# Kernel tuning notes

Measured on AMD Instinct MI355X. Metric: run time of the kernel, lower is better.

The kernel has to match this reference:

```python
import jax, jax.numpy as jnp
import numpy as np

HIDDEN = 4096
N_HEADS = 32
N_KV_HEADS = 8
HEAD_DIM = HIDDEN // N_HEADS  # 128
ROPE_THETA = 500000.0
B, S = 1, 2048


def setup_inputs() -> dict:
    key = jax.random.key(0)
    k1, k2, k3, k4, k5 = jax.random.split(key, 5)
    scale = 0.02
    return {
        "hidden_states": jax.random.normal(k1, (B, S, HIDDEN), dtype=jnp.float32),
        "Wq": jax.random.normal(k2, (N_HEADS * HEAD_DIM, HIDDEN), dtype=jnp.float32) * scale,
        "Wk": jax.random.normal(k3, (N_KV_HEADS * HEAD_DIM, HIDDEN), dtype=jnp.float32) * scale,
        "Wv": jax.random.normal(k4, (N_KV_HEADS * HEAD_DIM, HIDDEN), dtype=jnp.float32) * scale,
        "Wo": jax.random.normal(k5, (HIDDEN, N_HEADS * HEAD_DIM), dtype=jnp.float32) * scale,
    }


def _rope_cos_sin(seq_len, head_dim, theta, dtype):
    inv_freq = 1.0 / (theta ** (jnp.arange(0, head_dim, 2, dtype=jnp.float32) / head_dim))  # [hd/2]
    pos = jnp.arange(seq_len, dtype=jnp.float32)
    freqs = jnp.outer(pos, inv_freq)                      # [S, hd/2]
    emb = jnp.concatenate([freqs, freqs], axis=-1)        # [S, hd]
    return jnp.cos(emb).astype(dtype), jnp.sin(emb).astype(dtype)


def _rotate_half(x):
    x1, x2 = jnp.split(x, 2, axis=-1)
    return jnp.concatenate([-x2, x1], axis=-1)


def _apply_rope(x, cos, sin):
    # x: [B, H, S, hd]; cos/sin: [S, hd]
    return x * cos[None, None] + _rotate_half(x) * sin[None, None]


def reference(hidden_states, Wq, Wk, Wv, Wo):
    b, s, _ = hidden_states.shape
    groups = N_HEADS // N_KV_HEADS

    # fused QKV projections (Linear with weight [out, in])
    q = jnp.einsum("bsd,ed->bse", hidden_states, Wq).reshape(b, s, N_HEADS, HEAD_DIM).transpose(0, 2, 1, 3)
    k = jnp.einsum("bsd,ed->bse", hidden_states, Wk).reshape(b, s, N_KV_HEADS, HEAD_DIM).transpose(0, 2, 1, 3)
    v = jnp.einsum("bsd,ed->bse", hidden_states, Wv).reshape(b, s, N_KV_HEADS, HEAD_DIM).transpose(0, 2, 1, 3)

    cos, sin = _rope_cos_sin(s, HEAD_DIM, ROPE_THETA, hidden_states.dtype)
    q = _apply_rope(q, cos, sin)
    k = _apply_rope(k, cos, sin)

    # GQA: repeat kv heads across groups
    k = jnp.repeat(k, groups, axis=1)  # [B, N_HEADS, S, hd]
    v = jnp.repeat(v, groups, axis=1)

    scale = 1.0 / jnp.sqrt(jnp.asarray(HEAD_DIM, dtype=hidden_states.dtype))
    scores = jnp.einsum("bhqd,bhkd->bhqk", q, k) * scale  # [B, H, S, S]
    causal = jnp.tril(jnp.ones((s, s), dtype=bool))
    scores = jnp.where(causal[None, None], scores, jnp.asarray(-1e30, dtype=scores.dtype))
    attn = jax.nn.softmax(scores, axis=-1)

    out = jnp.einsum("bhqk,bhkd->bhqd", attn, v)          # [B, H, S, hd]
    out = out.transpose(0, 2, 1, 3).reshape(b, s, N_HEADS * HEAD_DIM)
    return jnp.einsum("bse,de->bsd", out, Wo)             # [B, S, HIDDEN]
```

## Files before the change

### kernel.cpp

```cpp
#include <hip/hip_runtime.h>

typedef __attribute__((ext_vector_type(8))) short bf16x8;
typedef __attribute__((ext_vector_type(4))) short bf16x4;
typedef __attribute__((ext_vector_type(4))) float f32x4;
typedef __attribute__((ext_vector_type(16))) float f32x16;

#define S_LEN  2048
#define HID    4096
#define NHEADS 32
#define NKVH   8
#define HDIM   128
#define QKVN   (HID + 2*NKVH*HDIM)
#define KOFS   HID
#define VOFS   (HID + NKVH*HDIM)

#define AS1 __attribute__((address_space(1)))
#define AS3 __attribute__((address_space(3)))

__device__ __forceinline__ unsigned short f2bf(float f){
  unsigned int x = __float_as_uint(f);
  x += 0x7fffu + ((x >> 16) & 1u);
  return (unsigned short)(x >> 16);
}
__device__ __forceinline__ float bf2f(unsigned short h){
  return __uint_as_float(((unsigned int)h) << 16);
}

__global__ void cvt_all(const float* __restrict__ hs, const float* __restrict__ wq,
                        const float* __restrict__ wk, const float* __restrict__ wv,
                        const float* __restrict__ wo,
                        unsigned short* __restrict__ Hb,
                        unsigned short* __restrict__ Wqkvb,
                        unsigned short* __restrict__ Wob){
  const int total = 12582912;
  for (int i = blockIdx.x * blockDim.x + threadIdx.x; i < total; i += gridDim.x * blockDim.x){
    const float* src; unsigned short* dst;
    if (i < 2097152)      { src = hs + (size_t)i*4;             dst = Hb    + (size_t)i*4; }
    else if (i < 6291456) { size_t l = i - 2097152;  src = wq + l*4; dst = Wqkvb + l*4; }
    else if (i < 7340032) { size_t l = i - 6291456;  src = wk + l*4; dst = Wqkvb + 16777216 + l*4; }
    else if (i < 8388608) { size_t l = i - 7340032;  src = wv + l*4; dst = Wqkvb + 20971520 + l*4; }
    else                  { size_t l = i - 8388608;  src = wo + l*4; dst = Wob   + l*4; }
    float4 v = *(const float4*)src;
    ushort4 o;
    o.x = f2bf(v.x); o.y = f2bf(v.y); o.z = f2bf(v.z); o.w = f2bf(v.w);
    *(ushort4*)dst = o;
  }
}

__global__ void rope_table(float* __restrict__ cosT, float* __restrict__ sinT){
  int idx = blockIdx.x * blockDim.x + threadIdx.x;
  int s = idx >> 6, i = idx & 63;
  float inv = expf(-(float)i * (13.122363377404329f / 64.0f));
  float a = (float)s * inv;
  cosT[idx] = cosf(a);
  sinT[idx] = sinf(a);
}

__global__ void rope_apply2(unsigned short* __restrict__ X, const float* __restrict__ cosT,
                            const float* __restrict__ sinT){
  const int totQ = S_LEN*NHEADS*64;
  const int total = totQ + S_LEN*NKVH*64;
  int idx = blockIdx.x * blockDim.x + threadIdx.x;
  if (idx >= total) return;
  int nh, colofs, local;
  if (idx < totQ){ nh = NHEADS; colofs = 0;    local = idx; }
  else           { nh = NKVH;   colofs = KOFS; local = idx - totQ; }
  int i = local & 63;
  int h = (local >> 6) % nh;
  int s = local / (64*nh);
  size_t base = (size_t)s*QKVN + colofs + h*HDIM + i;
  float x0 = bf2f(X[base]), x1 = bf2f(X[base+64]);
  float c = cosT[(s<<6)|i], sn = sinT[(s<<6)|i];
  X[base]    = f2bf(x0*c - x1*sn);
  X[base+64] = f2bf(x1*c + x0*sn);
}

__global__ __launch_bounds__(256) void transpose_v(const unsigned short* __restrict__ QKV,
                                                   unsigned short* __restrict__ Vt){
  __shared__ unsigned short T[64][130];
  const int qt = blockIdx.x, kvh = blockIdx.y;
  const int tid = threadIdx.x;
  #pragma unroll
  for (int i=0;i<4;i++){
    int c = tid + i*256;
    int sl = c >> 4;
    int d0 = (c & 15) * 8;
    bf16x8 v = *(const bf16x8*)&QKV[(size_t)(qt*64+sl)*QKVN + VOFS + kvh*HDIM + d0];
    #pragma unroll
    for (int j=0;j<8;j++) T[sl][d0+j] = (unsigned short)v[j];
  }
  __syncthreads();
  #pragma unroll
  for (int i=0;i<4;i++){
    int c = tid + i*256;
    int d = c >> 3;
    int p0 = (c & 7) * 8;
    bf16x8 o;
    #pragma unroll
    for (int j=0;j<8;j++) o[j] = (short)T[p0+j][d];
    *(bf16x8*)&Vt[((size_t)kvh*HDIM + d)*S_LEN + qt*64 + p0] = o;
  }
}

template<int BM, int BN, int WM, int WN, int OUTF32>
__global__ __launch_bounds__(256, 2) void gemm_fr(const unsigned short* __restrict__ A,
                                                  const unsigned short* __restrict__ W,
                                                  void* __restrict__ C, int M, int N, int K){
  constexpr int MF = (BM/WM)/16;
  constexpr int NF = (BN/WN)/16;
  constexpr int LA = BM/32;
  constexpr int LB = BN/32;
  constexpr int ABYTES = BM*128;
  constexpr int BBYTES = BN*128;
  __shared__ char lds_raw[2*ABYTES + 2*BBYTES];

  const int tid = threadIdx.x;
  const int lane = tid & 63, wv = tid >> 6;
  const int wm = wv / WN, wn = wv % WN;
  const int r = lane & 15, kq = lane >> 4;
  const int tn = blockIdx.x, tm = blockIdx.y;
  const unsigned short* Ab = A + (size_t)tm*BM*K;
  const unsigned short* Wb = W + (size_t)tn*BN*K;

  f32x4 acc[MF][NF];
  #pragma unroll
  for (int m=0;m<MF;m++)
    #pragma unroll
    for (int n=0;n<NF;n++) acc[m][n] = {0.f,0.f,0.f,0.f};

  auto swz = [](int row)->int { return ((row>>1)&3)<<1; };

  auto stage = [&](int buf, int kt){
    #pragma unroll
    for (int l=0;l<LA;l++){
      int c = l*256 + tid;
      int row = c >> 3, ch = c & 7;
      __builtin_amdgcn_global_load_lds(
        (const AS1 void*)(Ab + (size_t)row*K + kt + ((ch ^ swz(row))*8)),
        (AS3 void*)(lds_raw + buf*ABYTES + (l*256 + wv*64)*16), 16, 0, 0);
    }
    #pragma unroll
    for (int l=0;l<LB;l++){
      int c = l*256 + tid;
      int row = c >> 3, ch = c & 7;
      __builtin_amdgcn_global_load_lds(
        (const AS1 void*)(Wb + (size_t)row*K + kt + ((ch ^ swz(row))*8)),
        (AS3 void*)(lds_raw + 2*ABYTES + buf*BBYTES + (l*256 + wv*64)*16), 16, 0, 0);
    }
  };
  auto rdA = [&](int buf, int m, int kh)->bf16x8 {
    int row = wm*(BM/WM) + m*16 + r;
    int ch = (kh*4 + kq) ^ swz(row);
    return *(const bf16x8*)(lds_raw + buf*ABYTES + row*128 + ch*16);
  };
  auto rdB = [&](int buf, int n, int kh)->bf16x8 {
    int row = wn*(BN/WN) + n*16 + r;
    int ch = (kh*4 + kq) ^ swz(row);
    return *(const bf16x8*)(lds_raw + 2*ABYTES + buf*BBYTES + row*128 + ch*16);
  };

  const int nt = K/64;
  stage(0, 0);
  for (int t=0; t<nt; ++t){
    asm volatile("s_waitcnt vmcnt(0)" ::: "memory");
    __builtin_amdgcn_s_barrier();
    const int buf = t & 1;
    bf16x8 av0[MF], bv0[NF], av1[MF], bv1[NF];
    #pragma unroll
    for (int m=0;m<MF;m++) av0[m] = rdA(buf, m, 0);
    #pragma unroll
    for (int n=0;n<NF;n++) bv0[n] = rdB(buf, n, 0);
    #pragma unroll
    for (int m=0;m<MF;m++) av1[m] = rdA(buf, m, 1);
    #pragma unroll
    for (int n=0;n<NF;n++) bv1[n] = rdB(buf, n, 1);
    if (t+1 < nt) stage((t+1)&1, (t+1)*64);
    #pragma unroll
    for (int m=0;m<MF;m++)
      #pragma unroll
      for (int n=0;n<NF;n++)
        acc[m][n] = __builtin_amdgcn_mfma_f32_16x16x32_bf16(av0[m], bv0[n], acc[m][n], 0, 0, 0);
    #pragma unroll
    for (int m=0;m<MF;m++)
      #pragma unroll
      for (int n=0;n<NF;n++)
        acc[m][n] = __builtin_amdgcn_mfma_f32_16x16x32_bf16(av1[m], bv1[n], acc[m][n], 0, 0, 0);
  }

  #pragma unroll
  for (int m=0;m<MF;m++)
    #pragma unroll
    for (int n=0;n<NF;n++)
      #pragma unroll
      for (int j=0;j<4;j++){
        int gr = tm*BM + wm*(BM/WM) + m*16 + kq*4 + j;
        int gc = tn*BN + wn*(BN/WN) + n*16 + r;
        if (OUTF32) ((float*)C)[(size_t)gr*N + gc] = acc[m][n][j];
        else ((unsigned short*)C)[(size_t)gr*N + gc] = f2bf(acc[m][n][j]);
      }
}

__global__ __launch_bounds__(256, 2) void attn_fwd3(const unsigned short* __restrict__ QKV,
                                                    const unsigned short* __restrict__ Vt,
                                                    unsigned short* __restrict__ AO){
  __shared__ unsigned short Ks[2][64*128];
  __shared__ unsigned short Vs[2][128*64];
  __shared__ float Ls[4][32];
  const int tid = threadIdx.x;
  const int lane = tid & 63, wv = tid >> 6;
  const int bid = blockIdx.x;
  const int h = bid & 31;
  const int qt = (S_LEN/128 - 1) - (bid >> 5);
  const int kvh = h >> 2;
  const int qb = qt * 128;
  const int q0w = qb + wv * 32;
  const int l31 = lane & 31, g = lane >> 5;
  const int qg = q0w + l31;

  const float CS = 0.12751743f;
  const float C0 = 17.312340f;

  bf16x8 qf[8];
  #pragma unroll
  for (int st=0; st<8; ++st)
    qf[st] = *(const bf16x8*)&QKV[(size_t)qg*QKVN + h*HDIM + st*16 + g*8];

  f32x16 oacc[4];
  #pragma unroll
  for (int db=0; db<4; ++db)
    #pragma unroll
    for (int i=0;i<16;i++) oacc[db][i] = 0.f;
  float lsum = 0.f;

  const unsigned short* Kbase = QKV + KOFS + kvh*HDIM;
  const unsigned short* Vbase = Vt + (size_t)kvh*HDIM*S_LEN;

  auto stage = [&](int buf, int kv0){
    #pragma unroll
    for (int l=0; l<4; ++l){
      int c = l*256 + tid;
      int row = c >> 4, ch = c & 15;
      __builtin_amdgcn_global_load_lds(
        (const AS1 void*)(Kbase + (size_t)(kv0+row)*QKVN + ((ch ^ (row&15))*8)),
        (AS3 void*)((char*)&Ks[buf][0] + (l*256 + wv*64)*16), 16, 0, 0);
    }
    #pragma unroll
    for (int l=0; l<4; ++l){
      int c = l*256 + tid;
      int row = c >> 3, ch = c & 7;
      __builtin_amdgcn_global_load_lds(
        (const AS1 void*)(Vbase + (size_t)row*S_LEN + kv0 + ((ch ^ (row&7))*8)),
        (AS3 void*)((char*)&Vs[buf][0] + (l*256 + wv*64)*16), 16, 0, 0);
    }
  };

  const int nt = 2*qt + 2;
  stage(0, 0);
  for (int t=0; t<nt; ++t){
    __syncthreads();
    if (t+1 < nt) stage((t+1)&1, (t+1)*64);
    const int kv0 = t*64;
    if (kv0 > q0w + 31) continue;
    const unsigned short* K_ = &Ks[t&1][0];
    const unsigned short* V_ = &Vs[t&1][0];

    f32x16 a0, a1;
    #pragma unroll
    for (int i=0;i<16;i++){ a0[i]=0.f; a1[i]=0.f; }
    #pragma unroll
    for (int st=0; st<8; ++st){
      int ch = (2*st + g) ^ (l31 & 15);
      bf16x8 k0 = *(const bf16x8*)&K_[ l31*128      + ch*8 ];
      int ch1 = (2*st + g) ^ ((32+l31) & 15);
      bf16x8 k1 = *(const bf16x8*)&K_[ (32+l31)*128 + ch1*8 ];
      a0 = __builtin_amdgcn_mfma_f32_32x32x16_bf16(k0, qf[st], a0, 0,0,0);
      a1 = __builtin_amdgcn_mfma_f32_32x32x16_bf16(k1, qf[st], a1, 0,0,0);
    }

    float p0[16], p1[16];
    const bool dm = (kv0 + 63 > q0w);
    const int lim = qg - kv0 - 4*g;
    #pragma unroll
    for (int i=0;i<16;i++){
      const int co = (i&3) + 8*(i>>2);
      float e0 = fmaf(a0[i], CS, -C0);
      float e1 = fmaf(a1[i], CS, -C0);
      if (dm){
        if (co      > lim) e0 = -200.f;
        if (co + 32 > lim) e1 = -200.f;
      }
      p0[i] = exp2f(fminf(e0, 60.f));
      p1[i] = exp2f(fminf(e1, 60.f));
    }
    {
      float u0 = (p0[0]+p0[1])+(p0[2]+p0[3]);
      float u1 = (p0[4]+p0[5])+(p0[6]+p0[7]);
      float u2 = (p0[8]+p0[9])+(p0[10]+p0[11]);
      float u3 = (p0[12]+p0[13])+(p0[14]+p0[15]);
      float v0 = (p1[0]+p1[1])+(p1[2]+p1[3]);
      float v1 = (p1[4]+p1[5])+(p1[6]+p1[7]);
      float v2 = (p1[8]+p1[9])+(p1[10]+p1[11]);
      float v3 = (p1[12]+p1[13])+(p1[14]+p1[15]);
      lsum += ((u0+u1)+(u2+u3)) + ((v0+v1)+(v2+v3));
    }

    bf16x8 pa[4];
    #pragma unroll
    for (int u=0; u<4; ++u){
      const float* P = (u<2) ? p0 : p1;
      const int i0 = 8*(u&1);
      unsigned int w0,w1,w2,w3;
      asm("v_cvt_pk_bf16_f32 %0, %1, %2" : "=v"(w0) : "v"(P[i0+0]), "v"(P[i0+1]));
      asm("v_cvt_pk_bf16_f32 %0, %1, %2" : "=v"(w1) : "v"(P[i0+2]), "v"(P[i0+3]));
      asm("v_cvt_pk_bf16_f32 %0, %1, %2" : "=v"(w2) : "v"(P[i0+4]), "v"(P[i0+5]));
      asm("v_cvt_pk_bf16_f32 %0, %1, %2" : "=v"(w3) : "v"(P[i0+6]), "v"(P[i0+7]));
      unsigned int r0 = __shfl_xor(g ? w0 : w2, 32);
      unsigned int r1 = __shfl_xor(g ? w1 : w3, 32);
      union { unsigned int u4[4]; bf16x8 v; } pk;
      pk.u4[0] = g ? r0 : w0;
      pk.u4[1] = g ? r1 : w1;
      pk.u4[2] = g ? w2 : r0;
      pk.u4[3] = g ? w3 : r1;
      pa[u] = pk.v;
    }

    #pragma unroll
    for (int u=0; u<4; ++u)
      #pragma unroll
      for (int db=0; db<4; ++db){
        int row = db*32 + l31;
        int ch = (2*u + g) ^ (row & 7);
        bf16x8 vb = *(const bf16x8*)&V_[row*64 + ch*8];
        oacc[db] = __builtin_amdgcn_mfma_f32_32x32x16_bf16(pa[u], vb, oacc[db], 0,0,0);
      }
  }

  float ls = lsum + __shfl_xor(lsum, 32);
  float inv = 1.0f / fmaxf(ls, 1e-30f);
  Ls[wv][l31] = inv;
  #pragma unroll
  for (int ib=0; ib<4; ++ib){
    float4 iv = *(const float4*)&Ls[wv][8*ib + 4*g];
    float ivv[4] = {iv.x, iv.y, iv.z, iv.w};
    #pragma unroll
    for (int c3=0; c3<4; ++c3){
      int row = 8*ib + 4*g + c3;
      #pragma unroll
      for (int db=0; db<4; ++db){
        AO[(size_t)(qb + wv*32 + row)*HID + h*HDIM + db*32 + l31] =
          f2bf(oacc[db][4*ib+c3] * ivv[c3]);
      }
    }
  }
}

extern "C" void kernel_launch(void* const* d_in, const int* in_sizes, int n_in,
                              void* d_out, int out_size, void* d_ws, size_t ws_size,
                              hipStream_t stream){
  (void)in_sizes; (void)n_in; (void)out_size; (void)ws_size;
  const float* hs = (const float*)d_in[0];
  const float* Wq = (const float*)d_in[1];
  const float* Wk = (const float*)d_in[2];
  const float* Wv = (const float*)d_in[3];
  const float* Wo = (const float*)d_in[4];
  float* out = (float*)d_out;
  char* ws = (char*)d_ws;
  size_t off = 0;
  auto alloc = [&](size_t bytes)->void*{ void* p = ws + off; off += (bytes + 255) & ~(size_t)255; return p; };

  unsigned short* Hb    = (unsigned short*)alloc((size_t)S_LEN*HID*2);
  unsigned short* Wqkvb = (unsigned short*)alloc((size_t)QKVN*HID*2);
  unsigned short* Wob   = (unsigned short*)alloc((size_t)HID*HID*2);
  unsigned short* QKVb  = (unsigned short*)alloc((size_t)S_LEN*QKVN*2);
  unsigned short* AOb   = (unsigned short*)alloc((size_t)S_LEN*HID*2);
  unsigned short* Vtb   = (unsigned short*)alloc((size_t)NKVH*HDIM*S_LEN*2);
  float* cosT = (float*)alloc((size_t)S_LEN*64*4);
  float* sinT = (float*)alloc((size_t)S_LEN*64*4);

  cvt_all<<<2048, 256, 0, stream>>>(hs, Wq, Wk, Wv, Wo, Hb, Wqkvb, Wob);
  rope_table<<<(S_LEN*64)/256, 256, 0, stream>>>(cosT, sinT);

  gemm_fr<128,192,1,4,0><<<dim3(QKVN/192, S_LEN/128), 256, 0, stream>>>(Hb, Wqkvb, QKVb, S_LEN, QKVN, HID);

  transpose_v<<<dim3(S_LEN/64, NKVH), 256, 0, stream>>>(QKVb, Vtb);

  {
    int total = S_LEN*NHEADS*64 + S_LEN*NKVH*64;
    rope_apply2<<<(total+255)/256, 256, 0, stream>>>(QKVb, cosT, sinT);
  }

  attn_fwd3<<<dim3(512), 256, 0, stream>>>(QKVb, Vtb, AOb);

  gemm_fr<128,128,2,2,1><<<dim3(HID/128, S_LEN/128), 256, 0, stream>>>(AOb, Wob, out, S_LEN, HID, HID);
}
```

Measured before the change: 288.1 us.

## Load GEMM A operand directly from global memory, staging only B in LDS

New measurement: 446.1 us. 54.8% more time.

```diff
diff --git a/kernel.cpp b/kernel.cpp
--- a/kernel.cpp
+++ b/kernel.cpp
@@ -103,16 +103,14 @@
 }
 
 template<int BM, int BN, int WM, int WN, int OUTF32>
-__global__ __launch_bounds__(256, 2) void gemm_fr(const unsigned short* __restrict__ A,
-                                                  const unsigned short* __restrict__ W,
-                                                  void* __restrict__ C, int M, int N, int K){
+__global__ __launch_bounds__(256, 2) void gemm_flat(const unsigned short* __restrict__ A,
+                                                    const unsigned short* __restrict__ W,
+                                                    void* __restrict__ C, int M, int N, int K){
   constexpr int MF = (BM/WM)/16;
   constexpr int NF = (BN/WN)/16;
-  constexpr int LA = BM/32;
   constexpr int LB = BN/32;
-  constexpr int ABYTES = BM*128;
   constexpr int BBYTES = BN*128;
-  __shared__ char lds_raw[2*ABYTES + 2*BBYTES];
+  __shared__ char lds_raw[2*BBYTES];
 
   const int tid = threadIdx.x;
   const int lane = tid & 63, wv = tid >> 6;
@@ -121,6 +119,7 @@
   const int tn = blockIdx.x, tm = blockIdx.y;
   const unsigned short* Ab = A + (size_t)tm*BM*K;
   const unsigned short* Wb = W + (size_t)tn*BN*K;
+  const unsigned short* Alane = Ab + (size_t)(wm*(BM/WM) + r)*K + kq*8;
 
   f32x4 acc[MF][NF];
   #pragma unroll
@@ -130,51 +129,40 @@
 
   auto swz = [](int row)->int { return ((row>>1)&3)<<1; };
 
-  auto stage = [&](int buf, int kt){
-    #pragma unroll
-    for (int l=0;l<LA;l++){
-      int c = l*256 + tid;
-      int row = c >> 3, ch = c & 7;
-      __builtin_amdgcn_global_load_lds(
-        (const AS1 void*)(Ab + (size_t)row*K + kt + ((ch ^ swz(row))*8)),
-        (AS3 void*)(lds_raw + buf*ABYTES + (l*256 + wv*64)*16), 16, 0, 0);
-    }
+  auto stageB = [&](int buf, int kt){
     #pragma unroll
     for (int l=0;l<LB;l++){
       int c = l*256 + tid;
       int row = c >> 3, ch = c & 7;
       __builtin_amdgcn_global_load_lds(
         (const AS1 void*)(Wb + (size_t)row*K + kt + ((ch ^ swz(row))*8)),
-        (AS3 void*)(lds_raw + 2*ABYTES + buf*BBYTES + (l*256 + wv*64)*16), 16, 0, 0);
-    }
-  };
-  auto rdA = [&](int buf, int m, int kh)->bf16x8 {
-    int row = wm*(BM/WM) + m*16 + r;
-    int ch = (kh*4 + kq) ^ swz(row);
-    return *(const bf16x8*)(lds_raw + buf*ABYTES + row*128 + ch*16);
+        (AS3 void*)(lds_raw + buf*BBYTES + (l*256 + wv*64)*16), 16, 0, 0);
+    }
   };
   auto rdB = [&](int buf, int n, int kh)->bf16x8 {
     int row = wn*(BN/WN) + n*16 + r;
     int ch = (kh*4 + kq) ^ swz(row);
-    return *(const bf16x8*)(lds_raw + 2*ABYTES + buf*BBYTES + row*128 + ch*16);
+    return *(const bf16x8*)(lds_raw + buf*BBYTES + row*128 + ch*16);
   };
 
   const int nt = K/64;
-  stage(0, 0);
+  stageB(0, 0);
   for (int t=0; t<nt; ++t){
     asm volatile("s_waitcnt vmcnt(0)" ::: "memory");
     __builtin_amdgcn_s_barrier();
     const int buf = t & 1;
-    bf16x8 av0[MF], bv0[NF], av1[MF], bv1[NF];
-    #pragma unroll
-    for (int m=0;m<MF;m++) av0[m] = rdA(buf, m, 0);
+    const int kt = t*64;
+    bf16x8 av0[MF], av1[MF];
+    #pragma unroll
+    for (int m=0;m<MF;m++) av0[m] = *(const bf16x8*)(Alane + (size_t)(m*16)*K + kt);
+    #pragma unroll
+    for (int m=0;m<MF;m++) av1[m] = *(const bf16x8*)(Alane + (size_t)(m*16)*K + kt + 32);
+    if (t+1 < nt) stageB((t+1)&1, (t+1)*64);
+    bf16x8 bv0[NF], bv1[NF];
     #pragma unroll
     for (int n=0;n<NF;n++) bv0[n] = rdB(buf, n, 0);
     #pragma unroll
-    for (int m=0;m<MF;m++) av1[m] = rdA(buf, m, 1);
-    #pragma unroll
     for (int n=0;n<NF;n++) bv1[n] = rdB(buf, n, 1);
-    if (t+1 < nt) stage((t+1)&1, (t+1)*64);
     #pragma unroll
     for (int m=0;m<MF;m++)
       #pragma unroll
@@ -380,7 +368,7 @@
   cvt_all<<<2048, 256, 0, stream>>>(hs, Wq, Wk, Wv, Wo, Hb, Wqkvb, Wob);
   rope_table<<<(S_LEN*64)/256, 256, 0, stream>>>(cosT, sinT);
 
-  gemm_fr<128,192,1,4,0><<<dim3(QKVN/192, S_LEN/128), 256, 0, stream>>>(Hb, Wqkvb, QKVb, S_LEN, QKVN, HID);
+  gemm_flat<128,192,2,2,0><<<dim3(QKVN/192, S_LEN/128), 256, 0, stream>>>(Hb, Wqkvb, QKVb, S_LEN, QKVN, HID);
 
   transpose_v<<<dim3(S_LEN/64, NKVH), 256, 0, stream>>>(QKVb, Vtb);
 
@@ -391,5 +379,5 @@
 
   attn_fwd3<<<dim3(512), 256, 0, stream>>>(QKVb, Vtb, AOb);
 
-  gemm_fr<128,128,2,2,1><<<dim3(HID/128, S_LEN/128), 256, 0, stream>>>(AOb, Wob, out, S_LEN, HID, HID);
-}
+  gemm_flat<128,128,2,2,1><<<dim3(HID/128, S_LEN/128), 256, 0, stream>>>(AOb, Wob, out, S_LEN, HID, HID);
+}
```
